# Kernel optimization log

Hardware: AMD Instinct MI355X
Metric: run time of the kernel (lower is better)

The kernel has to match this reference:

```python
import jax, jax.numpy as jnp
import numpy as np

N, E = 100000, 400000
ATOM_DIM, HIDDEN, LAYERS, HEADS = 74, 256, 3, 4
OUT = HIDDEN // HEADS


def setup_inputs() -> dict:
    key = jax.random.key(0)
    ks = jax.random.split(key, 12)
    s = 1.0 / np.sqrt(HIDDEN)
    return {
        'atom_feat': jax.random.normal(ks[0], (N, ATOM_DIM), jnp.float32),
        'src': jax.random.randint(ks[1], (E,), 0, N, jnp.int32),
        'dst': jax.random.randint(ks[2], (E,), 0, N, jnp.int32),
        'W_in': jax.random.normal(ks[3], (ATOM_DIM, HIDDEN), jnp.float32) / np.sqrt(ATOM_DIM),
        'b_in': jnp.zeros((HIDDEN,), jnp.float32),
        'W_src': jax.random.normal(ks[4], (LAYERS, HIDDEN, HIDDEN), jnp.float32) * s,
        'b_src': jnp.zeros((LAYERS, HIDDEN), jnp.float32),
        'W_dst': jax.random.normal(ks[5], (LAYERS, HIDDEN, HIDDEN), jnp.float32) * s,
        'b_dst': jnp.zeros((LAYERS, HIDDEN), jnp.float32),
        'attn': jax.random.normal(ks[6], (LAYERS, HEADS, OUT), jnp.float32) * s,
        'bias': jnp.zeros((LAYERS, HIDDEN), jnp.float32),
    }


def _gatv2_layer(h, src, dst, Ws, bs, Wd, bd, a, b_out):
    # h: [N, HIDDEN]; fc_src / fc_dst projections reshaped to [N, HEADS, OUT]
    fs = (h @ Ws + bs).reshape(N, HEADS, OUT)
    fd = (h @ Wd + bd).reshape(N, HEADS, OUT)
    # GATv2: e_ij = a . leaky_relu(Ws h_i + Wd h_j) per head  -> [E, HEADS]
    e = jax.nn.leaky_relu(fs[src] + fd[dst], negative_slope=0.2)
    logits = jnp.einsum('ehd,hd->eh', e, a)
    # segment softmax over incoming edges of each dst node
    m = jax.ops.segment_max(logits, dst, num_segments=N)      # [N, HEADS]
    ex = jnp.exp(logits - m[dst])
    denom = jax.ops.segment_sum(ex, dst, num_segments=N)      # [N, HEADS]
    alpha = ex / denom[dst]                                   # [E, HEADS]
    # weighted scatter-aggregate of source features -> [N, HEADS, OUT]
    msg = alpha[:, :, None] * fs[src]
    rst = jax.ops.segment_sum(msg, dst, num_segments=N)
    # flatten(1) + per-layer output bias
    return rst.reshape(N, HIDDEN) + b_out


def reference(atom_feat, src, dst, W_in, b_in, W_src, b_src, W_dst, b_dst, attn, bias):
    h = atom_feat @ W_in + b_in
    for l in range(LAYERS):
        h = _gatv2_layer(h, src, dst, W_src[l], b_src[l], W_dst[l], b_dst[l], attn[l], bias[l])
    return h  # [N, HIDDEN]; per-molecule list is just slicing of this matrix
```

## Files before the change

kernel.cpp:

```cpp
#include <hip/hip_runtime.h>
#include <hip/hip_fp16.h>

#define HID   256
#define NHEAD 4
#define DOUT  64
#define ADIM  74
#define KPAD_IN 96
#define LAYERS 3

typedef _Float16 half8 __attribute__((ext_vector_type(8)));
typedef _Float16 half4 __attribute__((ext_vector_type(4)));
typedef float f32x4 __attribute__((ext_vector_type(4)));

__device__ __forceinline__ void gload16(const void* g, void* l) {
  __builtin_amdgcn_global_load_lds((const __attribute__((address_space(1))) void*)g,
                                   (__attribute__((address_space(3))) void*)l, 16, 0, 0);
}

__global__ void k_prep_wt(const float* __restrict__ Ws, const float* __restrict__ Wd,
                          _Float16* __restrict__ WT) {
  int l = blockIdx.y;
  int id = blockIdx.x * 256 + threadIdx.x;
  if (id >= 512 * HID) return;
  int n = id >> 8, k = id & 255;
  const float* W = (n < HID) ? (Ws + (size_t)l * HID * HID)
                             : (Wd + (size_t)l * HID * HID);
  int nn = (n < HID) ? n : (n - HID);
  WT[(size_t)l * 512 * HID + id] = (_Float16)W[k * HID + nn];
}

__global__ void k_prep_win(const float* __restrict__ Win, _Float16* __restrict__ WT) {
  int id = blockIdx.x * 256 + threadIdx.x;
  if (id >= HID * KPAD_IN) return;
  int n = id / KPAD_IN, k = id % KPAD_IN;
  WT[id] = (_Float16)((k < ADIM) ? Win[k * HID + n] : 0.f);
}

__device__ __forceinline__ void gemm_epilogue2(
    f32x4 acc[4][4], char* smem, int t, int lane, int wm, int wn,
    int row0, int col0, int M,
    const float* bias0, const float* bias1,
    _Float16* outS, _Float16* outD)
{
  const float* bp = (col0 < HID) ? (bias0 + col0) : (bias1 + (col0 - HID));
  _Float16*    op = (col0 < HID) ? (outS + col0) : (outD + (col0 - HID));
  _Float16 (*C)[136] = (_Float16(*)[136])smem;
  #pragma unroll
  for (int half = 0; half < 2; ++half) {
    __syncthreads();
    if (wm == half) {
      #pragma unroll
      for (int i = 0; i < 4; ++i) {
        #pragma unroll
        for (int j = 0; j < 4; ++j) {
          int lc = wn * 64 + j * 16 + (lane & 15);
          float bv = bp[lc];
          #pragma unroll
          for (int r = 0; r < 4; ++r) {
            int lr = i * 16 + (lane >> 4) * 4 + r;
            C[lr][lc] = (_Float16)(acc[i][j][r] + bv);
          }
        }
      }
    }
    __syncthreads();
    int lr = t >> 2, seg = t & 3;
    int grow = row0 + half * 64 + lr;
    if (grow < M) {
      const _Float16* sp = &C[lr][seg * 32];
      _Float16* dp = op + (size_t)grow * HID + seg * 32;
      #pragma unroll
      for (int q = 0; q < 4; ++q)
        *(uint4*)(dp + q * 8) = *(const uint4*)(sp + q * 8);
    }
  }
}

__global__ __launch_bounds__(256)
void k_gemm_h(const _Float16* __restrict__ A, int M,
              const _Float16* __restrict__ B,
              const float* __restrict__ bias0, const float* __restrict__ bias1,
              _Float16* __restrict__ outS, _Float16* __restrict__ outD)
{
  __shared__ __align__(16) char smem[49152];
  const int t = threadIdx.x, lane = t & 63, wid = t >> 6;
  const int wm = wid >> 1, wn = wid & 1;
  const int nwg = gridDim.x, id = blockIdx.x;
  const int qc = nwg >> 3, rc = nwg & 7, xcd = id & 7, idx = id >> 3;
  const int swz = (xcd < rc ? xcd * (qc + 1) : rc * (qc + 1) + (xcd - rc) * qc) + idx;
  const int col0 = (swz & 3) * 128, row0 = (swz >> 2) * 128;

  f32x4 acc[4][4];
  #pragma unroll
  for (int i = 0; i < 4; ++i)
    #pragma unroll
    for (int j = 0; j < 4; ++j)
      acc[i][j] = (f32x4){0.f, 0.f, 0.f, 0.f};

  auto stage = [&](int kt, int buf) {
    const int kb = kt * 32;
    char* Ab = smem + buf * 16384;
    char* Bb = Ab + 8192;
    #pragma unroll
    for (int q = 0; q < 2; ++q) {
      int ci = wid * 2 + q;
      int lr = lane >> 2;
      int r = ci * 16 + lr;
      int slot = (lane & 3) ^ ((lr >> 1) & 3);
      int grow = row0 + r; grow = grow < M ? grow : (M - 1);
      gload16(A + (size_t)grow * HID + kb + slot * 8, Ab + ci * 1024);
      gload16(B + (size_t)(col0 + r) * HID + kb + slot * 8, Bb + ci * 1024);
    }
  };

  stage(0, 0);
  stage(1, 1);
  const int slot_off = (((lane >> 4) ^ ((lane >> 1) & 3)) << 4);
  const int ar0 = (wm * 64 + (lane & 15)) * 64 + slot_off;
  const int br0 = (wn * 64 + (lane & 15)) * 64 + slot_off;

  #pragma unroll
  for (int kt = 0; kt < 8; ++kt) {
    if (kt + 2 < 8) stage(kt + 2, (kt + 2) % 3);
    if (kt < 6)       asm volatile("s_waitcnt vmcnt(8)" ::: "memory");
    else if (kt == 6) asm volatile("s_waitcnt vmcnt(4)" ::: "memory");
    else              asm volatile("s_waitcnt vmcnt(0)" ::: "memory");
    __builtin_amdgcn_s_barrier();
    __builtin_amdgcn_sched_barrier(0);
    const char* Ab = smem + (kt % 3) * 16384;
    const char* Bb = Ab + 8192;
    half8 af[4], bf[4];
    #pragma unroll
    for (int i = 0; i < 4; ++i) af[i] = *(const half8*)(Ab + ar0 + i * 1024);
    #pragma unroll
    for (int j = 0; j < 4; ++j) bf[j] = *(const half8*)(Bb + br0 + j * 1024);
    __builtin_amdgcn_s_setprio(1);
    #pragma unroll
    for (int i = 0; i < 4; ++i)
      #pragma unroll
      for (int j = 0; j < 4; ++j)
        acc[i][j] = __builtin_amdgcn_mfma_f32_16x16x32_f16(af[i], bf[j], acc[i][j], 0, 0, 0);
    __builtin_amdgcn_s_setprio(0);
    asm volatile("s_waitcnt lgkmcnt(0)" ::: "memory");
    __builtin_amdgcn_sched_barrier(0);
    __builtin_amdgcn_s_barrier();
    __builtin_amdgcn_sched_barrier(0);
  }
  gemm_epilogue2(acc, smem, t, lane, wm, wn, row0, col0, M, bias0, bias1, outS, outD);
}

__global__ __launch_bounds__(256)
void k_gemm_f(const float* __restrict__ A, int M,
              const _Float16* __restrict__ B,
              const float* __restrict__ bias0,
              _Float16* __restrict__ outS)
{
  __shared__ __align__(16) char smem[17408];
  const int t = threadIdx.x, lane = t & 63, wid = t >> 6;
  const int wm = wid >> 1, wn = wid & 1;
  const int nwg = gridDim.x, id = blockIdx.x;
  const int qc = nwg >> 3, rc = nwg & 7, xcd = id & 7, idx = id >> 3;
  const int swz = (xcd < rc ? xcd * (qc + 1) : rc * (qc + 1) + (xcd - rc) * qc) + idx;
  const int col0 = (swz & 1) * 128, row0 = (swz >> 1) * 128;
  char* Ab = smem;
  char* Bb = smem + 8192;

  f32x4 acc[4][4];
  #pragma unroll
  for (int i = 0; i < 4; ++i)
    #pragma unroll
    for (int j = 0; j < 4; ++j)
      acc[i][j] = (f32x4){0.f, 0.f, 0.f, 0.f};

  const int slot_off = (((lane >> 4) ^ ((lane >> 1) & 3)) << 4);
  const int ar0 = (wm * 64 + (lane & 15)) * 64 + slot_off;
  const int br0 = (wn * 64 + (lane & 15)) * 64 + slot_off;

  for (int kt = 0; kt < 3; ++kt) {
    const int kb = kt * 32;
    #pragma unroll
    for (int it = 0; it < 4; ++it) {
      int idx2 = t + it * 256;
      int r = idx2 >> 3, c4 = idx2 & 7;
      int gr = row0 + r;
      int k0 = kb + c4 * 4;
      float x0 = 0.f, x1 = 0.f, x2 = 0.f, x3 = 0.f;
      if (gr < M) {
        const float* ap = A + (size_t)gr * ADIM;
        if (k0 + 0 < ADIM) x0 = ap[k0 + 0];
        if (k0 + 1 < ADIM) x1 = ap[k0 + 1];
        if (k0 + 2 < ADIM) x2 = ap[k0 + 2];
        if (k0 + 3 < ADIM) x3 = ap[k0 + 3];
      }
      half4 hv = {(_Float16)x0, (_Float16)x1, (_Float16)x2, (_Float16)x3};
      int off = r * 64 + ((((c4 >> 1) ^ ((r >> 1) & 3)) << 4)) + (c4 & 1) * 8;
      *(half4*)(Ab + off) = hv;
    }
    #pragma unroll
    for (int q = 0; q < 2; ++q) {
      int ci = wid * 2 + q;
      int lr = lane >> 2;
      int r = ci * 16 + lr;
      int slot = (lane & 3) ^ ((lr >> 1) & 3);
      gload16(B + (size_t)(col0 + r) * KPAD_IN + kb + slot * 8, Bb + ci * 1024);
    }
    __syncthreads();
    half8 af[4], bf[4];
    #pragma unroll
    for (int i = 0; i < 4; ++i) af[i] = *(const half8*)(Ab + ar0 + i * 1024);
    #pragma unroll
    for (int j = 0; j < 4; ++j) bf[j] = *(const half8*)(Bb + br0 + j * 1024);
    #pragma unroll
    for (int i = 0; i < 4; ++i)
      #pragma unroll
      for (int j = 0; j < 4; ++j)
        acc[i][j] = __builtin_amdgcn_mfma_f32_16x16x32_f16(af[i], bf[j], acc[i][j], 0, 0, 0);
    __syncthreads();
  }
  gemm_epilogue2(acc, smem, t, lane, wm, wn, row0, col0, M, bias0, bias0, outS, outS);
}

__global__ __launch_bounds__(256)
void k_fused(const int* __restrict__ offs, const int* __restrict__ esrc,
             const int* __restrict__ perm,
             const _Float16* __restrict__ fs, const _Float16* __restrict__ fd,
             const float* __restrict__ attn, const float* __restrict__ bias,
             _Float16* __restrict__ hhalf, float* __restrict__ hfloat, int N)
{
  int gid = blockIdx.x * 8 + (threadIdx.x >> 5);
  if (gid >= N) return;
  int n = perm[gid];
  int sub = threadIdx.x & 31;
  int h = sub >> 3;
  int j0 = sub * 8;
  half8 fdv = *(const half8*)&fd[(size_t)n * HID + j0];
  float4 av0 = *(const float4*)&attn[h * DOUT + (sub & 7) * 8];
  float4 av1 = *(const float4*)&attn[h * DOUT + (sub & 7) * 8 + 4];
  float4 bv0 = *(const float4*)&bias[j0];
  float4 bv1 = *(const float4*)&bias[j0 + 4];
  float fdf[8], avf[8], bvf[8];
  #pragma unroll
  for (int q = 0; q < 4; ++q) {
    avf[q] = ((const float*)&av0)[q]; avf[q + 4] = ((const float*)&av1)[q];
    bvf[q] = ((const float*)&bv0)[q]; bvf[q + 4] = ((const float*)&bv1)[q];
  }
  #pragma unroll
  for (int q = 0; q < 8; ++q) fdf[q] = (float)fdv[q];

  int t0 = offs[n], t1 = offs[n + 1];
  float m = -1e30f, ssum = 0.f;
  float a[8];
  #pragma unroll
  for (int q = 0; q < 8; ++q) a[q] = 0.f;

  half8 fA = {}, fB = {};
  if (t0 < t1)     fA = *(const half8*)&fs[(size_t)esrc[t0] * HID + j0];
  if (t0 + 1 < t1) fB = *(const half8*)&fs[(size_t)esrc[t0 + 1] * HID + j0];
  int tt = t0;
  for (; tt + 1 < t1; tt += 2) {
    float fa[8], fb[8];
    #pragma unroll
    for (int q = 0; q < 8; ++q) { fa[q] = (float)fA[q]; fb[q] = (float)fB[q]; }
    if (tt + 2 < t1) fA = *(const half8*)&fs[(size_t)esrc[tt + 2] * HID + j0];
    if (tt + 3 < t1) fB = *(const half8*)&fs[(size_t)esrc[tt + 3] * HID + j0];
    float pa = 0.f, pb = 0.f;
    #pragma unroll
    for (int q = 0; q < 8; ++q) {
      float xa = fa[q] + fdf[q]; xa = xa > 0.f ? xa : 0.2f * xa; pa += xa * avf[q];
      float xb = fb[q] + fdf[q]; xb = xb > 0.f ? xb : 0.2f * xb; pb += xb * avf[q];
    }
    pa += __shfl_xor(pa, 1); pb += __shfl_xor(pb, 1);
    pa += __shfl_xor(pa, 2); pb += __shfl_xor(pb, 2);
    pa += __shfl_xor(pa, 4); pb += __shfl_xor(pb, 4);
    float mx = fmaxf(m, fmaxf(pa, pb));
    float sc = __expf(m - mx);
    float wa = __expf(pa - mx);
    float wb = __expf(pb - mx);
    ssum = ssum * sc + wa + wb;
    #pragma unroll
    for (int q = 0; q < 8; ++q) a[q] = a[q] * sc + wa * fa[q] + wb * fb[q];
    m = mx;
  }
  if (tt < t1) {
    float fa[8];
    #pragma unroll
    for (int q = 0; q < 8; ++q) fa[q] = (float)fA[q];
    float pa = 0.f;
    #pragma unroll
    for (int q = 0; q < 8; ++q) {
      float xa = fa[q] + fdf[q]; xa = xa > 0.f ? xa : 0.2f * xa; pa += xa * avf[q];
    }
    pa += __shfl_xor(pa, 1);
    pa += __shfl_xor(pa, 2);
    pa += __shfl_xor(pa, 4);
    float mx = fmaxf(m, pa);
    float sc = __expf(m - mx);
    float wa = __expf(pa - mx);
    ssum = ssum * sc + wa;
    #pragma unroll
    for (int q = 0; q < 8; ++q) a[q] = a[q] * sc + wa * fa[q];
    m = mx;
  }
  float inv = (t1 > t0) ? 1.0f / ssum : 0.f;
  float o[8];
  #pragma unroll
  for (int q = 0; q < 8; ++q) o[q] = a[q] * inv + bvf[q];
  if (hhalf) {
    half8 hv;
    #pragma unroll
    for (int q = 0; q < 8; ++q) hv[q] = (_Float16)o[q];
    *(half8*)&hhalf[(size_t)n * HID + j0] = hv;
  }
  if (hfloat) {
    float4 v0 = {o[0], o[1], o[2], o[3]};
    float4 v1 = {o[4], o[5], o[6], o[7]};
    *(float4*)&hfloat[(size_t)n * HID + j0] = v0;
    *(float4*)&hfloat[(size_t)n * HID + j0 + 4] = v1;
  }
}

__global__ void k_zero_i(int* p, int n) {
  int i = blockIdx.x * 256 + threadIdx.x;
  if (i < n) p[i] = 0;
}
__global__ void k_count(const int* __restrict__ dst, int* __restrict__ counts, int E) {
  int i = blockIdx.x * 256 + threadIdx.x;
  if (i < E) atomicAdd(&counts[dst[i]], 1);
}
__global__ __launch_bounds__(1024)
void k_scan1(const int* __restrict__ counts, int* __restrict__ offs,
             int* __restrict__ bsums, int* __restrict__ dhist, int N)
{
  __shared__ int sd[1024];
  __shared__ int hh[64];
  int t = threadIdx.x, i = blockIdx.x * 1024 + t;
  if (t < 64) hh[t] = 0;
  int x = (i < N) ? counts[i] : 0;
  sd[t] = x;
  __syncthreads();
  if (i < N) atomicAdd(&hh[x < 63 ? x : 63], 1);
  for (int off = 1; off < 1024; off <<= 1) {
    int v = (t >= off) ? sd[t - off] : 0;
    __syncthreads();
    sd[t] += v;
    __syncthreads();
  }
  if (i < N) offs[i] = sd[t] - x;
  if (t == 0) bsums[blockIdx.x] = sd[1023];
  __syncthreads();
  if (t < 64 && hh[t] > 0) atomicAdd(&dhist[t], hh[t]);
}
__global__ void k_scan2(const int* __restrict__ bsums, int* __restrict__ boffs,
                        int* __restrict__ offs, int nb, int N)
{
  if (threadIdx.x == 0 && blockIdx.x == 0) {
    int run = 0;
    for (int b = 0; b < nb; ++b) { boffs[b] = run; run += bsums[b]; }
    offs[N] = run;
  }
}
__global__ void k_deg_scan(const int* __restrict__ dhist, int* __restrict__ dcur) {
  int t = threadIdx.x;
  int x = dhist[t];
  int sum = x;
  for (int off = 1; off < 64; off <<= 1) {
    int v = __shfl_up(sum, off);
    if (t >= off) sum += v;
  }
  dcur[t] = sum - x;
}
__global__ __launch_bounds__(1024)
void k_scan3(const int* __restrict__ boffs, int* __restrict__ offs,
             int* __restrict__ cursor, int N)
{
  int i = blockIdx.x * 1024 + threadIdx.x;
  if (i < N) {
    int v = offs[i] + boffs[blockIdx.x];
    offs[i] = v;
    cursor[i] = v;
  }
}
__global__ void k_scatter(const int* __restrict__ src, const int* __restrict__ dst,
                          int* __restrict__ cursor, int* __restrict__ esrc, int E)
{
  int i = blockIdx.x * 256 + threadIdx.x;
  if (i < E) {
    int pos = atomicAdd(&cursor[dst[i]], 1);
    esrc[pos] = src[i];
  }
}
__global__ __launch_bounds__(256)
void k_deg_scatter(const int* __restrict__ counts, int* __restrict__ dcur,
                   int* __restrict__ perm, int N)
{
  __shared__ int hist[64];
  __shared__ int base[64];
  int t = threadIdx.x;
  int i = blockIdx.x * 256 + t;
  if (t < 64) hist[t] = 0;
  __syncthreads();
  int d = 0, lrank = 0;
  if (i < N) {
    d = counts[i]; d = d < 63 ? d : 63;
    lrank = atomicAdd(&hist[d], 1);
  }
  __syncthreads();
  if (t < 64 && hist[t] > 0) base[t] = atomicAdd(&dcur[t], hist[t]);
  __syncthreads();
  if (i < N) perm[base[d] + lrank] = i;
}

extern "C" void kernel_launch(void* const* d_in, const int* in_sizes, int n_in,
                              void* d_out, int out_size, void* d_ws, size_t ws_size,
                              hipStream_t stream)
{
  const float* atom  = (const float*)d_in[0];
  const int*   src   = (const int*)d_in[1];
  const int*   dst   = (const int*)d_in[2];
  const float* W_in  = (const float*)d_in[3];
  const float* b_in  = (const float*)d_in[4];
  const float* W_src = (const float*)d_in[5];
  const float* b_src = (const float*)d_in[6];
  const float* W_dst = (const float*)d_in[7];
  const float* b_dst = (const float*)d_in[8];
  const float* attn  = (const float*)d_in[9];
  const float* bias  = (const float*)d_in[10];

  const int N = in_sizes[0] / ADIM;
  const int E = in_sizes[1];
  _Float16* h_half = (_Float16*)d_out;
  float*    h_out  = (float*)d_out;

  char* w = (char*)d_ws;
  size_t off = 0;
  auto carve = [&](size_t bytes) {
    void* p = w + off;
    off = (off + bytes + 255) & ~(size_t)255;
    return p;
  };
  _Float16* fs    = (_Float16*)carve((size_t)N * HID * 2);
  _Float16* fd    = (_Float16*)carve((size_t)N * HID * 2);
  _Float16* WT    = (_Float16*)carve((size_t)LAYERS * 512 * HID * 2);
  _Float16* WTin  = (_Float16*)carve((size_t)HID * KPAD_IN * 2);
  int*      counts= (int*)carve((size_t)(N + 64) * 4);
  int*      dhist = counts + N;
  int*      offs  = (int*)carve((size_t)(N + 1) * 4);
  int*      cursor= (int*)carve((size_t)N * 4);
  int*      esrc  = (int*)carve((size_t)E * 4);
  int*      perm  = (int*)carve((size_t)N * 4);
  int*      dcur  = (int*)carve((size_t)64 * 4);
  int*      bsums = (int*)carve((size_t)1024 * 4);
  int*      boffs = (int*)carve((size_t)1024 * 4);
  (void)ws_size; (void)n_in; (void)out_size;

  const int nb = (N + 1023) / 1024;
  const int gmx = (N + 127) / 128;

  k_zero_i<<<(N + 64 + 255) / 256, 256, 0, stream>>>(counts, N + 64);
  k_count<<<(E + 255) / 256, 256, 0, stream>>>(dst, counts, E);
  k_scan1<<<nb, 1024, 0, stream>>>(counts, offs, bsums, dhist, N);
  k_scan2<<<1, 64, 0, stream>>>(bsums, boffs, offs, nb, N);
  k_deg_scan<<<1, 64, 0, stream>>>(dhist, dcur);
  k_scan3<<<nb, 1024, 0, stream>>>(boffs, offs, cursor, N);
  k_scatter<<<(E + 255) / 256, 256, 0, stream>>>(src, dst, cursor, esrc, E);
  k_deg_scatter<<<(N + 255) / 256, 256, 0, stream>>>(counts, dcur, perm, N);

  k_prep_win<<<(HID * KPAD_IN + 255) / 256, 256, 0, stream>>>(W_in, WTin);
  k_prep_wt<<<dim3((512 * HID + 255) / 256, LAYERS), 256, 0, stream>>>(W_src, W_dst, WT);
  k_gemm_f<<<2 * gmx, 256, 0, stream>>>(atom, N, WTin, b_in, h_half);

  for (int l = 0; l < LAYERS; ++l) {
    k_gemm_h<<<4 * gmx, 256, 0, stream>>>(h_half, N, WT + (size_t)l * 512 * HID,
                                          b_src + (size_t)l * HID,
                                          b_dst + (size_t)l * HID, fs, fd);
    const bool last = (l == LAYERS - 1);
    k_fused<<<(N + 7) / 8, 256, 0, stream>>>(offs, esrc, perm, fs, fd,
                                             attn + (size_t)l * NHEAD * DOUT,
                                             bias + (size_t)l * HID,
                                             last ? nullptr : h_half,
                                             last ? h_out : nullptr, N);
  }
}
```

Baseline: 459.8 us.

## Load GEMM operands directly from global memory into registers, dropping LDS pipeline

The hidden-state projection GEMM no longer stages A/B tiles through a triple-buffered LDS pipeline with barriers. Each lane instead reads its MFMA fragments straight from global memory, relying on cache for reuse. LDS shrinks to what the epilogue needs and launch bounds now request 3 blocks per CU to raise occupancy. The trade is more global/L2 traffic, since fragments are no longer shared across waves, and no explicit prefetch overlap.

```diff
diff --git a/kernel.cpp b/kernel.cpp
--- a/kernel.cpp
+++ b/kernel.cpp
@@ -76,13 +76,13 @@
   }
 }
 
-__global__ __launch_bounds__(256)
+__global__ __launch_bounds__(256, 3)
 void k_gemm_h(const _Float16* __restrict__ A, int M,
               const _Float16* __restrict__ B,
               const float* __restrict__ bias0, const float* __restrict__ bias1,
               _Float16* __restrict__ outS, _Float16* __restrict__ outD)
 {
-  __shared__ __align__(16) char smem[49152];
+  __shared__ __align__(16) char smem[17408];
   const int t = threadIdx.x, lane = t & 63, wid = t >> 6;
   const int wm = wid >> 1, wn = wid & 1;
   const int nwg = gridDim.x, id = blockIdx.x;
@@ -97,54 +97,33 @@
     for (int j = 0; j < 4; ++j)
       acc[i][j] = (f32x4){0.f, 0.f, 0.f, 0.f};
 
-  auto stage = [&](int kt, int buf) {
-    const int kb = kt * 32;
-    char* Ab = smem + buf * 16384;
-    char* Bb = Ab + 8192;
-    #pragma unroll
-    for (int q = 0; q < 2; ++q) {
-      int ci = wid * 2 + q;
-      int lr = lane >> 2;
-      int r = ci * 16 + lr;
-      int slot = (lane & 3) ^ ((lr >> 1) & 3);
-      int grow = row0 + r; grow = grow < M ? grow : (M - 1);
-      gload16(A + (size_t)grow * HID + kb + slot * 8, Ab + ci * 1024);
-      gload16(B + (size_t)(col0 + r) * HID + kb + slot * 8, Bb + ci * 1024);
-    }
-  };
-
-  stage(0, 0);
-  stage(1, 1);
-  const int slot_off = (((lane >> 4) ^ ((lane >> 1) & 3)) << 4);
-  const int ar0 = (wm * 64 + (lane & 15)) * 64 + slot_off;
-  const int br0 = (wn * 64 + (lane & 15)) * 64 + slot_off;
+  const int koff = (lane >> 4) * 8;
+  const _Float16* apt[4];
+  const _Float16* bpt[4];
+  #pragma unroll
+  for (int i = 0; i < 4; ++i) {
+    int r = row0 + wm * 64 + i * 16 + (lane & 15);
+    r = r < M ? r : (M - 1);
+    apt[i] = A + (size_t)r * HID + koff;
+  }
+  #pragma unroll
+  for (int j = 0; j < 4; ++j) {
+    int c = col0 + wn * 64 + j * 16 + (lane & 15);
+    bpt[j] = B + (size_t)c * HID + koff;
+  }
 
   #pragma unroll
   for (int kt = 0; kt < 8; ++kt) {
-    if (kt + 2 < 8) stage(kt + 2, (kt + 2) % 3);
-    if (kt < 6)       asm volatile("s_waitcnt vmcnt(8)" ::: "memory");
-    else if (kt == 6) asm volatile("s_waitcnt vmcnt(4)" ::: "memory");
-    else              asm volatile("s_waitcnt vmcnt(0)" ::: "memory");
-    __builtin_amdgcn_s_barrier();
-    __builtin_amdgcn_sched_barrier(0);
-    const char* Ab = smem + (kt % 3) * 16384;
-    const char* Bb = Ab + 8192;
     half8 af[4], bf[4];
     #pragma unroll
-    for (int i = 0; i < 4; ++i) af[i] = *(const half8*)(Ab + ar0 + i * 1024);
-    #pragma unroll
-    for (int j = 0; j < 4; ++j) bf[j] = *(const half8*)(Bb + br0 + j * 1024);
-    __builtin_amdgcn_s_setprio(1);
+    for (int i = 0; i < 4; ++i) af[i] = *(const half8*)(apt[i] + kt * 32);
+    #pragma unroll
+    for (int j = 0; j < 4; ++j) bf[j] = *(const half8*)(bpt[j] + kt * 32);
     #pragma unroll
     for (int i = 0; i < 4; ++i)
       #pragma unroll
       for (int j = 0; j < 4; ++j)
         acc[i][j] = __builtin_amdgcn_mfma_f32_16x16x32_f16(af[i], bf[j], acc[i][j], 0, 0, 0);
-    __builtin_amdgcn_s_setprio(0);
-    asm volatile("s_waitcnt lgkmcnt(0)" ::: "memory");
-    __builtin_amdgcn_sched_barrier(0);
-    __builtin_amdgcn_s_barrier();
-    __builtin_amdgcn_sched_barrier(0);
   }
   gemm_epilogue2(acc, smem, t, lane, wm, wn, row0, col0, M, bias0, bias1, outS, outD);
 }
```

After: 614.3 us. +33.6%, slower.
